# Kernel optimization log

Hardware: AMD Instinct MI355X
Metric: run time of the kernel (lower is better)

Reference implementation:

```python
import jax, jax.numpy as jnp
import numpy as np

N, E, G = 50000, 1600000, 64
F_NODE, F_EDGE, ACT = 128, 16, 10
NEG_SLOPE = 0.2  # GATv2Conv default negative_slope
LAYER_DIMS = [(F_NODE, 32), (32, 64), (64, 128)]


def _glorot(k, shape):
    fan_in, fan_out = shape[0], shape[-1]
    s = jnp.sqrt(6.0 / (fan_in + fan_out))
    return jax.random.uniform(k, shape, jnp.float32, -s, s)


def setup_inputs() -> dict:
    key = jax.random.key(0)
    ks = iter(jax.random.split(key, 64))
    inp = {
        "x": jax.random.normal(next(ks), (N, F_NODE), jnp.float32),
        "edge_attr": jax.random.normal(next(ks), (E, F_EDGE), jnp.float32),
        "edge_index": jax.random.randint(next(ks), (2, E), 0, N, jnp.int32),
        "batch": jnp.sort(jax.random.randint(next(ks), (N,), 0, G, jnp.int32)),
    }
    for i, (din, dout) in enumerate(LAYER_DIMS, 1):
        inp[f"Wl{i}"] = _glorot(next(ks), (din, dout))   # lin_l (source transform)
        inp[f"bl{i}"] = jnp.zeros((dout,), jnp.float32)
        inp[f"Wr{i}"] = _glorot(next(ks), (din, dout))   # lin_r (dest transform)
        inp[f"br{i}"] = jnp.zeros((dout,), jnp.float32)
        inp[f"We{i}"] = _glorot(next(ks), (F_EDGE, dout))  # lin_edge (no bias)
        inp[f"att{i}"] = _glorot(next(ks), (1, dout))[0]   # attention vector
        inp[f"bo{i}"] = jnp.zeros((dout,), jnp.float32)    # output bias
    inp["Wv1"] = _glorot(next(ks), (128, 64)); inp["bv1"] = jnp.zeros((64,), jnp.float32)
    inp["Wv2"] = _glorot(next(ks), (64, 1));   inp["bv2"] = jnp.zeros((1,), jnp.float32)
    inp["Wa1"] = _glorot(next(ks), (128, 64)); inp["ba1"] = jnp.zeros((64,), jnp.float32)
    inp["Wa2"] = _glorot(next(ks), (64, ACT)); inp["ba2"] = jnp.zeros((ACT,), jnp.float32)
    return inp


def _gatv2(x, src, dst, ea, Wl, bl, Wr, br, We, att, bo):
    """GATv2Conv, heads=1, concat=True, edge_dim=F_EDGE (eval mode)."""
    xl = x @ Wl + bl                               # [N, D] source-side
    xr = x @ Wr + br                               # [N, D] dest-side
    m = xl[src] + xr[dst] + ea @ We                # [E, D]
    score = (jax.nn.leaky_relu(m, NEG_SLOPE) * att).sum(-1)  # [E]
    # segment softmax over edges grouped by destination node
    mx = jax.lax.stop_gradient(jax.ops.segment_max(score, dst, num_segments=N))
    ex = jnp.exp(score - mx[dst])
    den = jax.ops.segment_sum(ex, dst, num_segments=N)
    alpha = ex / (den[dst] + 1e-16)                # [E]
    out = jax.ops.segment_sum(alpha[:, None] * xl[src], dst, num_segments=N)
    return out + bo


def _forward(x, edge_attr, src, dst, batch, p):
    h = x
    for i in (1, 2, 3):
        h = jax.nn.relu(_gatv2(h, src, dst, edge_attr,
                               p[f"Wl{i}"], p[f"bl{i}"], p[f"Wr{i}"], p[f"br{i}"],
                               p[f"We{i}"], p[f"att{i}"], p[f"bo{i}"]))
    # global mean pool per graph
    cnt = jax.ops.segment_sum(jnp.ones((N,), h.dtype), batch, num_segments=G)
    pooled = jax.ops.segment_sum(h, batch, num_segments=G) / jnp.maximum(cnt, 1.0)[:, None]
    # dueling heads
    v = jax.nn.relu(pooled @ p["Wv1"] + p["bv1"]) @ p["Wv2"] + p["bv2"]      # [G, 1]
    a = jax.nn.relu(pooled @ p["Wa1"] + p["ba1"]) @ p["Wa2"] + p["ba2"]      # [G, ACT]
    return v + (a - a.mean(axis=1, keepdims=True))


def reference(x, edge_attr, edge_index, batch,
              Wl1, bl1, Wr1, br1, We1, att1, bo1,
              Wl2, bl2, Wr2, br2, We2, att2, bo2,
              Wl3, bl3, Wr3, br3, We3, att3, bo3,
              Wv1, bv1, Wv2, bv2, Wa1, ba1, Wa2, ba2):
    p = dict(Wl1=Wl1, bl1=bl1, Wr1=Wr1, br1=br1, We1=We1, att1=att1, bo1=bo1,
             Wl2=Wl2, bl2=bl2, Wr2=Wr2, br2=br2, We2=We2, att2=att2, bo2=bo2,
             Wl3=Wl3, bl3=bl3, Wr3=Wr3, br3=br3, We3=We3, att3=att3, bo3=bo3,
             Wv1=Wv1, bv1=bv1, Wv2=Wv2, bv2=bv2, Wa1=Wa1, ba1=ba1, Wa2=Wa2, ba2=ba2)
    return _forward(x, edge_attr, edge_index[0], edge_index[1], batch, p)
```

## Files before the change

### kernel.cpp

```cpp
#include <hip/hip_runtime.h>
#include <cstdint>
#include <cstddef>

static constexpr int NN = 50000;
static constexpr int NE = 1600000;
static constexpr int NG = 64;
static constexpr int FE = 16;

typedef float f32x4 __attribute__((ext_vector_type(4)));

template<int DIN, int DOUT>
__global__ __launch_bounds__(256) void k_node_linear(
    const float* __restrict__ h,
    const float* __restrict__ Wl, const float* __restrict__ bl,
    const float* __restrict__ Wr, const float* __restrict__ br,
    float* __restrict__ xl, float* __restrict__ xr)
{
    __shared__ float sW[2 * DIN * DOUT];
    __shared__ float sX[16 * DIN];
    const int n0 = blockIdx.x * 16;

    for (int i = threadIdx.x; i < DIN * DOUT; i += 256) {
        sW[i] = Wl[i];
        sW[DIN * DOUT + i] = Wr[i];
    }
    for (int i = threadIdx.x; i < 16 * DIN; i += 256) {
        int r = i / DIN, k = i % DIN;
        int n = n0 + r;
        sX[i] = (n < NN) ? h[(size_t)n * DIN + k] : 0.0f;
    }
    __syncthreads();

    for (int o = threadIdx.x; o < 16 * DOUT; o += 256) {
        int r = o / DOUT, d = o % DOUT;
        int n = n0 + r;
        if (n >= NN) continue;
        float accl = bl[d], accr = br[d];
        #pragma unroll 8
        for (int k = 0; k < DIN; ++k) {
            float xv = sX[r * DIN + k];
            accl = fmaf(xv, sW[k * DOUT + d], accl);
            accr = fmaf(xv, sW[DIN * DOUT + k * DOUT + d], accr);
        }
        xl[(size_t)n * DOUT + d] = accl;
        xr[(size_t)n * DOUT + d] = accr;
    }
}

__global__ __launch_bounds__(256) void k_count(
    const int* __restrict__ ei, int* __restrict__ cnt)
{
    const int e = blockIdx.x * 256 + threadIdx.x;
    if (e >= NE) return;
    atomicAdd(cnt + ei[NE + e], 1);
}

__global__ __launch_bounds__(1024) void k_scan(
    const int* __restrict__ cnt, int* __restrict__ rowptr)
{
    __shared__ int part[1024];
    const int T = 1024;
    const int C = (NN + T - 1) / T;
    const int t = threadIdx.x;
    const int base = t * C;
    int s = 0;
    for (int i = 0; i < C; ++i) {
        int idx = base + i;
        if (idx < NN) s += cnt[idx];
    }
    part[t] = s;
    __syncthreads();
    for (int off = 1; off < T; off <<= 1) {
        int v = 0;
        if (t >= off) v = part[t - off];
        __syncthreads();
        if (t >= off) part[t] += v;
        __syncthreads();
    }
    int run = (t == 0) ? 0 : part[t - 1];
    for (int i = 0; i < C; ++i) {
        int idx = base + i;
        if (idx < NN) { rowptr[idx] = run; run += cnt[idx]; }
    }
    if (t == T - 1) rowptr[NN] = run;
}

__global__ __launch_bounds__(256) void k_fill(
    const int* __restrict__ ei, const int* __restrict__ rowptr,
    int* __restrict__ woff, int* __restrict__ eids, int* __restrict__ esrc,
    const float* __restrict__ ea, float* __restrict__ eaperm, const int do_perm)
{
    const int e = blockIdx.x * 256 + threadIdx.x;
    if (e >= NE) return;
    const int dst = ei[NE + e];
    const int pos = rowptr[dst] + atomicAdd(woff + dst, 1);
    esrc[pos] = ei[e];
    if (do_perm) {
        const f32x4* s4 = (const f32x4*)(ea + (size_t)e * FE);
        f32x4* d4 = (f32x4*)(eaperm + (size_t)pos * FE);
        d4[0] = s4[0]; d4[1] = s4[1]; d4[2] = s4[2]; d4[3] = s4[3];
    } else {
        eids[pos] = e;
    }
}

template<int D, bool PERM>
__global__ __launch_bounds__(128, 4) void k_gat_fused(
    const int* __restrict__ rowptr, const int* __restrict__ eidx,
    const int* __restrict__ esrc, const float* __restrict__ eaf,
    const float* __restrict__ xl, const float* __restrict__ xr,
    const float* __restrict__ We, const float* __restrict__ att,
    const float* __restrict__ bo, float* __restrict__ hout)
{
    constexpr int SW  = D / 2;
    constexpr int EPW = 64 / SW;
    constexpr int WPB = 2;

    const int wave = threadIdx.x >> 6;
    const int lane = threadIdx.x & 63;
    const int n = blockIdx.x * WPB + wave;
    if (n >= NN) return;
    const int sub = lane / SW;
    const int dl  = lane % SW;
    const int d0  = 2 * dl;

    float rWe[2 * FE], rAtt[2], rXr[2], acc[2];
    {
        const float2 a2 = *(const float2*)(att + d0);
        rAtt[0] = a2.x; rAtt[1] = a2.y;
        const float2 x2 = *(const float2*)(xr + (size_t)n * D + d0);
        rXr[0] = x2.x; rXr[1] = x2.y;
        #pragma unroll
        for (int k = 0; k < FE; ++k) {
            const float2 w2 = *(const float2*)(We + k * D + d0);
            rWe[2 * k] = w2.x; rWe[2 * k + 1] = w2.y;
        }
        acc[0] = acc[1] = 0.f;
    }

    const int p0 = rowptr[n], p1 = rowptr[n + 1];
    float m = -3.4e38f, l = 0.f;

    auto load_edge = [&](int p, float (&eav)[FE], float (&rXl)[2]) {
        const int s = esrc[p];
        const float2 x2 = *(const float2*)(xl + (size_t)s * D + d0);
        rXl[0] = x2.x; rXl[1] = x2.y;
        int erow; if constexpr (PERM) erow = p; else erow = eidx[p];
        if constexpr (SW == 64) {
            const float* ep = eaf + (size_t)(unsigned)__builtin_amdgcn_readfirstlane(erow) * FE;
            #pragma unroll
            for (int k = 0; k < FE; ++k) eav[k] = ep[k];
        } else {
            const float* ep = eaf + (size_t)erow * FE;
            #pragma unroll
            for (int k4 = 0; k4 < 4; ++k4) {
                const float4 v = *(const float4*)(ep + 4 * k4);
                eav[4 * k4]     = v.x; eav[4 * k4 + 1] = v.y;
                eav[4 * k4 + 2] = v.z; eav[4 * k4 + 3] = v.w;
            }
        }
    };
    auto score_edge = [&](const float (&eav)[FE], const float (&rXl)[2]) -> float {
        float m0 = rXl[0] + rXr[0], m1 = rXl[1] + rXr[1];
        #pragma unroll
        for (int k = 0; k < FE; ++k) {
            m0 = fmaf(eav[k], rWe[2 * k], m0);
            m1 = fmaf(eav[k], rWe[2 * k + 1], m1);
        }
        m0 = fmaxf(m0, 0.2f * m0);
        m1 = fmaxf(m1, 0.2f * m1);
        float sv = fmaf(m0, rAtt[0], m1 * rAtt[1]);
        #pragma unroll
        for (int off = 1; off < SW; off <<= 1) sv += __shfl_xor(sv, off);
        return sv;
    };
    auto sm_update = [&](float sv, const float (&rXl)[2]) {
        const float dd = sv - m;
        float wexp;
        if (__builtin_expect(dd > 8.f, 0)) {
            const float r = __expf(-dd);
            acc[0] *= r; acc[1] *= r;
            l *= r; m = sv; wexp = 1.f;
        } else {
            wexp = __expf(dd);
        }
        acc[0] = fmaf(wexp, rXl[0], acc[0]);
        acc[1] = fmaf(wexp, rXl[1], acc[1]);
        l += wexp;
    };

    int p = p0 + sub;
    for (; p + EPW < p1; p += 2 * EPW) {
        float eavA[FE], rXlA[2], eavB[FE], rXlB[2];
        load_edge(p, eavA, rXlA);
        load_edge(p + EPW, eavB, rXlB);
        const float svA = score_edge(eavA, rXlA);
        const float svB = score_edge(eavB, rXlB);
        sm_update(svA, rXlA);
        sm_update(svB, rXlB);
    }
    if (p < p1) {
        float eav[FE], rXl[2];
        load_edge(p, eav, rXl);
        sm_update(score_edge(eav, rXl), rXl);
    }

    #pragma unroll
    for (int step = SW; step < 64; step <<= 1) {
        const float mo = __shfl_xor(m, step);
        const float mstar = fmaxf(m, mo);
        const float sc = __expf(m - mstar);
        acc[0] *= sc; acc[1] *= sc; l *= sc;
        acc[0] += __shfl_xor(acc[0], step);
        acc[1] += __shfl_xor(acc[1], step);
        l += __shfl_xor(l, step);
        m = mstar;
    }

    if (lane < SW) {
        const float inv = 1.0f / (l + 1e-16f);
        const float2 b2 = *(const float2*)(bo + d0);
        float2 o;
        o.x = fmaxf(fmaf(acc[0], inv, b2.x), 0.f);
        o.y = fmaxf(fmaf(acc[1], inv, b2.y), 0.f);
        *(float2*)(hout + (size_t)n * D + d0) = o;
    }
}

__global__ __launch_bounds__(128) void k_pool(
    const float* __restrict__ h, const int* __restrict__ batch,
    float* __restrict__ pooled, float* __restrict__ cnt)
{
    constexpr int BLOCKS = 512;
    constexpr int CH = (NN + BLOCKS - 1) / BLOCKS;
    const int t = threadIdx.x;
    const int n0 = blockIdx.x * CH;
    const int n1 = min(NN, n0 + CH);
    if (n0 >= n1) return;

    int g = batch[n0];
    float acc = 0.f, c = 0.f;
    for (int n = n0; n < n1; ++n) {
        const int bg = batch[n];
        if (bg != g) {
            atomicAdd(pooled + g * 128 + t, acc);
            if (t == 0) atomicAdd(cnt + g, c);
            acc = 0.f; c = 0.f; g = bg;
        }
        acc += h[(size_t)n * 128 + t];
        c += 1.f;
    }
    atomicAdd(pooled + g * 128 + t, acc);
    if (t == 0) atomicAdd(cnt + g, c);
}

__global__ __launch_bounds__(128) void k_head(
    const float* __restrict__ pooled, const float* __restrict__ cnt,
    const float* __restrict__ Wv1, const float* __restrict__ bv1,
    const float* __restrict__ Wv2, const float* __restrict__ bv2,
    const float* __restrict__ Wa1, const float* __restrict__ ba1,
    const float* __restrict__ Wa2, const float* __restrict__ ba2,
    float* __restrict__ out)
{
    __shared__ float pr[128];
    __shared__ float hv[64];
    __shared__ float ha[64];
    __shared__ float sA[10];
    __shared__ float sVM[2];
    const int g = blockIdx.x;
    const int t = threadIdx.x;

    const float inv = 1.0f / fmaxf(cnt[g], 1.0f);
    pr[t] = pooled[g * 128 + t] * inv;
    __syncthreads();

    if (t < 64) {
        float sv = bv1[t], sa = ba1[t];
        #pragma unroll 8
        for (int k = 0; k < 128; ++k) {
            float p = pr[k];
            sv = fmaf(p, Wv1[k * 64 + t], sv);
            sa = fmaf(p, Wa1[k * 64 + t], sa);
        }
        hv[t] = fmaxf(sv, 0.0f);
        ha[t] = fmaxf(sa, 0.0f);
    }
    __syncthreads();

    if (t < 10) {
        float av = ba2[t];
        #pragma unroll
        for (int j = 0; j < 64; ++j) av = fmaf(ha[j], Wa2[j * 10 + t], av);
        sA[t] = av;
    }
    if (t == 64) {
        float v = bv2[0];
        #pragma unroll
        for (int j = 0; j < 64; ++j) v = fmaf(hv[j], Wv2[j], v);
        sVM[0] = v;
    }
    __syncthreads();

    if (t == 0) {
        float s = 0.0f;
        #pragma unroll
        for (int j = 0; j < 10; ++j) s += sA[j];
        sVM[1] = s * 0.1f;
    }
    __syncthreads();

    if (t < 10) out[g * 10 + t] = sVM[0] + sA[t] - sVM[1];
}

extern "C" void kernel_launch(void* const* d_in, const int* in_sizes, int n_in,
                              void* d_out, int out_size, void* d_ws, size_t ws_size,
                              hipStream_t stream)
{
    const float* x     = (const float*)d_in[0];
    const float* ea    = (const float*)d_in[1];
    const int*   ei    = (const int*)d_in[2];
    const int*   batch = (const int*)d_in[3];

    float* ws = (float*)d_ws;
    float* xl     = ws;
    float* xr     = xl + (size_t)NN * 128;
    float* hA     = xr + (size_t)NN * 128;
    float* hB     = hA + (size_t)NN * 128;
    float* pooled = hB + (size_t)NN * 64;
    float* cntp   = pooled + (size_t)NG * 128;
    int*   rowptr = (int*)(cntp + NG);
    int*   cnt    = rowptr + (NN + 1);
    int*   woff   = cnt + NN;
    int*   eids   = woff + NN;
    int*   esrc   = eids + NE;
    float* eaperm = (float*)(esrc + NE);

    const size_t need = ((char*)(eaperm + (size_t)NE * FE)) - (char*)d_ws;
    const bool use_perm = (ws_size >= need);

    const int EB = (NE + 255) / 256;

    hipMemsetAsync(cnt, 0, 2 * NN * sizeof(int), stream);
    k_count<<<dim3(EB), dim3(256), 0, stream>>>(ei, cnt);
    k_scan<<<dim3(1), dim3(1024), 0, stream>>>(cnt, rowptr);
    k_fill<<<dim3(EB), dim3(256), 0, stream>>>(
        ei, rowptr, woff, eids, esrc, ea, eaperm, use_perm ? 1 : 0);

    const int GB = (NN + 1) / 2;

#define LAYER(DIN, DOUT, HIN, HOUT, B)                                                   \
    do {                                                                                 \
        k_node_linear<DIN, DOUT><<<dim3((NN + 15) / 16), dim3(256), 0, stream>>>(        \
            HIN, (const float*)d_in[B], (const float*)d_in[(B) + 1],                     \
            (const float*)d_in[(B) + 2], (const float*)d_in[(B) + 3], xl, xr);           \
        if (use_perm)                                                                    \
            k_gat_fused<DOUT, true><<<dim3(GB), dim3(128), 0, stream>>>(                 \
                rowptr, eids, esrc, eaperm, xl, xr, (const float*)d_in[(B) + 4],         \
                (const float*)d_in[(B) + 5], (const float*)d_in[(B) + 6], HOUT);         \
        else                                                                             \
            k_gat_fused<DOUT, false><<<dim3(GB), dim3(128), 0, stream>>>(                \
                rowptr, eids, esrc, ea, xl, xr, (const float*)d_in[(B) + 4],             \
                (const float*)d_in[(B) + 5], (const float*)d_in[(B) + 6], HOUT);         \
    } while (0)

    LAYER(128, 32, x,  hA, 4);
    LAYER(32,  64, hA, hB, 11);
    LAYER(64, 128, hB, hA, 18);

#undef LAYER

    hipMemsetAsync(pooled, 0, (NG * 128 + NG) * sizeof(float), stream);
    k_pool<<<dim3(512), dim3(128), 0, stream>>>(hA, batch, pooled, cntp);
    k_head<<<dim3(NG), dim3(128), 0, stream>>>(
        pooled, cntp,
        (const float*)d_in[25], (const float*)d_in[26],
        (const float*)d_in[27], (const float*)d_in[28],
        (const float*)d_in[29], (const float*)d_in[30],
        (const float*)d_in[31], (const float*)d_in[32],
        (float*)d_out);
}
```

Baseline: 1.003 ms.

## Drop edge-attr permutation, use packed FMA in GAT and vectorized node linear

Removes the permuted copy of edge attributes, so the GAT kernel always gathers edge attributes through edge ids from the original array. The edge score math is rewritten with 2-wide vector multiplies intended to map to packed FMA, and the manual two-edge unrolling is replaced by a simple loop with a waves-per-eu hint. The node linear kernel now computes four output columns per thread using 4-wide shared-memory loads. This saves a 100MB permutation write and its readback, but makes the three GAT layers do scattered reads of edge attributes instead of contiguous ones, and gives up the explicit load overlap from the unrolled loop.

New measurement: 1.210 ms. 1.21x slower.

```diff
diff --git a/kernel.cpp b/kernel.cpp
--- a/kernel.cpp
+++ b/kernel.cpp
@@ -7,6 +7,7 @@
 static constexpr int NG = 64;
 static constexpr int FE = 16;
 
+typedef float f32x2 __attribute__((ext_vector_type(2)));
 typedef float f32x4 __attribute__((ext_vector_type(4)));
 
 template<int DIN, int DOUT>
@@ -31,19 +32,21 @@
     }
     __syncthreads();
 
-    for (int o = threadIdx.x; o < 16 * DOUT; o += 256) {
-        int r = o / DOUT, d = o % DOUT;
-        int n = n0 + r;
+    constexpr int NQ = DOUT / 4;
+    for (int o = threadIdx.x; o < 16 * NQ; o += 256) {
+        const int r = o / NQ, d0 = 4 * (o % NQ);
+        const int n = n0 + r;
         if (n >= NN) continue;
-        float accl = bl[d], accr = br[d];
-        #pragma unroll 8
+        f32x4 accl = *(const f32x4*)(bl + d0);
+        f32x4 accr = *(const f32x4*)(br + d0);
+        #pragma unroll 4
         for (int k = 0; k < DIN; ++k) {
-            float xv = sX[r * DIN + k];
-            accl = fmaf(xv, sW[k * DOUT + d], accl);
-            accr = fmaf(xv, sW[DIN * DOUT + k * DOUT + d], accr);
-        }
-        xl[(size_t)n * DOUT + d] = accl;
-        xr[(size_t)n * DOUT + d] = accr;
+            const float xv = sX[r * DIN + k];
+            accl += xv * *(const f32x4*)(sW + k * DOUT + d0);
+            accr += xv * *(const f32x4*)(sW + DIN * DOUT + k * DOUT + d0);
+        }
+        *(f32x4*)(xl + (size_t)n * DOUT + d0) = accl;
+        *(f32x4*)(xr + (size_t)n * DOUT + d0) = accr;
     }
 }
 
@@ -87,25 +90,20 @@
 
 __global__ __launch_bounds__(256) void k_fill(
     const int* __restrict__ ei, const int* __restrict__ rowptr,
-    int* __restrict__ woff, int* __restrict__ eids, int* __restrict__ esrc,
-    const float* __restrict__ ea, float* __restrict__ eaperm, const int do_perm)
+    int* __restrict__ woff, int* __restrict__ eids, int* __restrict__ esrc)
 {
     const int e = blockIdx.x * 256 + threadIdx.x;
     if (e >= NE) return;
     const int dst = ei[NE + e];
     const int pos = rowptr[dst] + atomicAdd(woff + dst, 1);
+    eids[pos] = e;
     esrc[pos] = ei[e];
-    if (do_perm) {
-        const f32x4* s4 = (const f32x4*)(ea + (size_t)e * FE);
-        f32x4* d4 = (f32x4*)(eaperm + (size_t)pos * FE);
-        d4[0] = s4[0]; d4[1] = s4[1]; d4[2] = s4[2]; d4[3] = s4[3];
-    } else {
-        eids[pos] = e;
-    }
-}
-
-template<int D, bool PERM>
-__global__ __launch_bounds__(128, 4) void k_gat_fused(
+}
+
+template<int D>
+__global__ __launch_bounds__(128)
+__attribute__((amdgpu_waves_per_eu(2, 4)))
+void k_gat_fused(
     const int* __restrict__ rowptr, const int* __restrict__ eidx,
     const int* __restrict__ esrc, const float* __restrict__ eaf,
     const float* __restrict__ xl, const float* __restrict__ xr,
@@ -114,95 +112,78 @@
 {
     constexpr int SW  = D / 2;
     constexpr int EPW = 64 / SW;
-    constexpr int WPB = 2;
 
     const int wave = threadIdx.x >> 6;
     const int lane = threadIdx.x & 63;
-    const int n = blockIdx.x * WPB + wave;
+    const int n = blockIdx.x * 2 + wave;
     if (n >= NN) return;
     const int sub = lane / SW;
     const int dl  = lane % SW;
     const int d0  = 2 * dl;
 
-    float rWe[2 * FE], rAtt[2], rXr[2], acc[2];
-    {
-        const float2 a2 = *(const float2*)(att + d0);
-        rAtt[0] = a2.x; rAtt[1] = a2.y;
-        const float2 x2 = *(const float2*)(xr + (size_t)n * D + d0);
-        rXr[0] = x2.x; rXr[1] = x2.y;
-        #pragma unroll
-        for (int k = 0; k < FE; ++k) {
-            const float2 w2 = *(const float2*)(We + k * D + d0);
-            rWe[2 * k] = w2.x; rWe[2 * k + 1] = w2.y;
-        }
-        acc[0] = acc[1] = 0.f;
-    }
-
+    f32x2 WeP0[FE / 2], WeP1[FE / 2];
+    #pragma unroll
+    for (int j = 0; j < FE / 2; ++j) {
+        const float2 a2 = *(const float2*)(We + (2 * j) * D + d0);
+        const float2 b2 = *(const float2*)(We + (2 * j + 1) * D + d0);
+        WeP0[j] = (f32x2){a2.x, b2.x};
+        WeP1[j] = (f32x2){a2.y, b2.y};
+    }
+    const float2 rAtt = *(const float2*)(att + d0);
+    const float2 rXr  = *(const float2*)(xr + (size_t)n * D + d0);
+
+    float acc0 = 0.f, acc1 = 0.f, m = -3.4e38f, l = 0.f;
     const int p0 = rowptr[n], p1 = rowptr[n + 1];
-    float m = -3.4e38f, l = 0.f;
-
-    auto load_edge = [&](int p, float (&eav)[FE], float (&rXl)[2]) {
+
+    for (int p = p0 + sub; p < p1; p += EPW) {
         const int s = esrc[p];
-        const float2 x2 = *(const float2*)(xl + (size_t)s * D + d0);
-        rXl[0] = x2.x; rXl[1] = x2.y;
-        int erow; if constexpr (PERM) erow = p; else erow = eidx[p];
+        const int erow = eidx[p];
+        const float2 xl2 = *(const float2*)(xl + (size_t)s * D + d0);
+
+        f32x2 ep[FE / 2];
         if constexpr (SW == 64) {
-            const float* ep = eaf + (size_t)(unsigned)__builtin_amdgcn_readfirstlane(erow) * FE;
+            const float* epp = eaf + (size_t)(unsigned)__builtin_amdgcn_readfirstlane(erow) * FE;
             #pragma unroll
-            for (int k = 0; k < FE; ++k) eav[k] = ep[k];
+            for (int j = 0; j < FE / 2; ++j)
+                ep[j] = (f32x2){epp[2 * j], epp[2 * j + 1]};
         } else {
-            const float* ep = eaf + (size_t)erow * FE;
+            const f32x4* ep4 = (const f32x4*)(eaf + (size_t)erow * FE);
             #pragma unroll
-            for (int k4 = 0; k4 < 4; ++k4) {
-                const float4 v = *(const float4*)(ep + 4 * k4);
-                eav[4 * k4]     = v.x; eav[4 * k4 + 1] = v.y;
-                eav[4 * k4 + 2] = v.z; eav[4 * k4 + 3] = v.w;
+            for (int j4 = 0; j4 < 4; ++j4) {
+                const f32x4 v = ep4[j4];
+                ep[2 * j4]     = (f32x2){v.x, v.y};
+                ep[2 * j4 + 1] = (f32x2){v.z, v.w};
             }
         }
-    };
-    auto score_edge = [&](const float (&eav)[FE], const float (&rXl)[2]) -> float {
-        float m0 = rXl[0] + rXr[0], m1 = rXl[1] + rXr[1];
-        #pragma unroll
-        for (int k = 0; k < FE; ++k) {
-            m0 = fmaf(eav[k], rWe[2 * k], m0);
-            m1 = fmaf(eav[k], rWe[2 * k + 1], m1);
-        }
+
+        f32x2 q0 = WeP0[0] * ep[0];
+        f32x2 q1 = WeP1[0] * ep[0];
+        #pragma unroll
+        for (int j = 1; j < FE / 2; ++j) {
+            q0 += WeP0[j] * ep[j];
+            q1 += WeP1[j] * ep[j];
+        }
+
+        float m0 = (xl2.x + rXr.x) + (q0.x + q0.y);
+        float m1 = (xl2.y + rXr.y) + (q1.x + q1.y);
         m0 = fmaxf(m0, 0.2f * m0);
         m1 = fmaxf(m1, 0.2f * m1);
-        float sv = fmaf(m0, rAtt[0], m1 * rAtt[1]);
+        float sv = fmaf(m0, rAtt.x, m1 * rAtt.y);
         #pragma unroll
         for (int off = 1; off < SW; off <<= 1) sv += __shfl_xor(sv, off);
-        return sv;
-    };
-    auto sm_update = [&](float sv, const float (&rXl)[2]) {
+
         const float dd = sv - m;
         float wexp;
         if (__builtin_expect(dd > 8.f, 0)) {
             const float r = __expf(-dd);
-            acc[0] *= r; acc[1] *= r;
+            acc0 *= r; acc1 *= r;
             l *= r; m = sv; wexp = 1.f;
         } else {
             wexp = __expf(dd);
         }
-        acc[0] = fmaf(wexp, rXl[0], acc[0]);
-        acc[1] = fmaf(wexp, rXl[1], acc[1]);
+        acc0 = fmaf(wexp, xl2.x, acc0);
+        acc1 = fmaf(wexp, xl2.y, acc1);
         l += wexp;
-    };
-
-    int p = p0 + sub;
-    for (; p + EPW < p1; p += 2 * EPW) {
-        float eavA[FE], rXlA[2], eavB[FE], rXlB[2];
-        load_edge(p, eavA, rXlA);
-        load_edge(p + EPW, eavB, rXlB);
-        const float svA = score_edge(eavA, rXlA);
-        const float svB = score_edge(eavB, rXlB);
-        sm_update(svA, rXlA);
-        sm_update(svB, rXlB);
-    }
-    if (p < p1) {
-        float eav[FE], rXl[2];
-        load_edge(p, eav, rXl);
-        sm_update(score_edge(eav, rXl), rXl);
     }
 
     #pragma unroll
@@ -210,9 +191,9 @@
         const float mo = __shfl_xor(m, step);
         const float mstar = fmaxf(m, mo);
         const float sc = __expf(m - mstar);
-        acc[0] *= sc; acc[1] *= sc; l *= sc;
-        acc[0] += __shfl_xor(acc[0], step);
-        acc[1] += __shfl_xor(acc[1], step);
+        acc0 *= sc; acc1 *= sc; l *= sc;
+        acc0 += __shfl_xor(acc0, step);
+        acc1 += __shfl_xor(acc1, step);
         l += __shfl_xor(l, step);
         m = mstar;
     }
@@ -221,8 +202,8 @@
         const float inv = 1.0f / (l + 1e-16f);
         const float2 b2 = *(const float2*)(bo + d0);
         float2 o;
-        o.x = fmaxf(fmaf(acc[0], inv, b2.x), 0.f);
-        o.y = fmaxf(fmaf(acc[1], inv, b2.y), 0.f);
+        o.x = fmaxf(fmaf(acc0, inv, b2.x), 0.f);
+        o.y = fmaxf(fmaf(acc1, inv, b2.y), 0.f);
         *(float2*)(hout + (size_t)n * D + d0) = o;
     }
 }
@@ -333,18 +314,13 @@
     int*   woff   = cnt + NN;
     int*   eids   = woff + NN;
     int*   esrc   = eids + NE;
-    float* eaperm = (float*)(esrc + NE);
-
-    const size_t need = ((char*)(eaperm + (size_t)NE * FE)) - (char*)d_ws;
-    const bool use_perm = (ws_size >= need);
 
     const int EB = (NE + 255) / 256;
 
     hipMemsetAsync(cnt, 0, 2 * NN * sizeof(int), stream);
     k_count<<<dim3(EB), dim3(256), 0, stream>>>(ei, cnt);
     k_scan<<<dim3(1), dim3(1024), 0, stream>>>(cnt, rowptr);
-    k_fill<<<dim3(EB), dim3(256), 0, stream>>>(
-        ei, rowptr, woff, eids, esrc, ea, eaperm, use_perm ? 1 : 0);
+    k_fill<<<dim3(EB), dim3(256), 0, stream>>>(ei, rowptr, woff, eids, esrc);
 
     const int GB = (NN + 1) / 2;
 
@@ -353,14 +329,9 @@
         k_node_linear<DIN, DOUT><<<dim3((NN + 15) / 16), dim3(256), 0, stream>>>(        \
             HIN, (const float*)d_in[B], (const float*)d_in[(B) + 1],                     \
             (const float*)d_in[(B) + 2], (const float*)d_in[(B) + 3], xl, xr);           \
-        if (use_perm)                                                                    \
-            k_gat_fused<DOUT, true><<<dim3(GB), dim3(128), 0, stream>>>(                 \
-                rowptr, eids, esrc, eaperm, xl, xr, (const float*)d_in[(B) + 4],         \
-                (const float*)d_in[(B) + 5], (const float*)d_in[(B) + 6], HOUT);         \
-        else                                                                             \
-            k_gat_fused<DOUT, false><<<dim3(GB), dim3(128), 0, stream>>>(                \
-                rowptr, eids, esrc, ea, xl, xr, (const float*)d_in[(B) + 4],             \
-                (const float*)d_in[(B) + 5], (const float*)d_in[(B) + 6], HOUT);         \
+        k_gat_fused<DOUT><<<dim3(GB), dim3(128), 0, stream>>>(                           \
+            rowptr, eids, esrc, ea, xl, xr, (const float*)d_in[(B) + 4],                 \
+            (const float*)d_in[(B) + 5], (const float*)d_in[(B) + 6], HOUT);             \
     } while (0)
 
     LAYER(128, 32, x,  hA, 4);
```
